# Optimization experiments

Measured on AMD Instinct MI355X. Metric: run time of the kernel, lower is better.

Reference implementation:

```python
import jax, jax.numpy as jnp
import numpy as np

EPS = 1e-7


def _project_to_ball(x, max_norm=0.9):
    # keep points strictly inside the unit Poincare ball
    n = jnp.linalg.norm(x, axis=-1, keepdims=True)
    return x * (max_norm / (1.0 + n))


def _poincare_pairwise_dist(x, y, c=1.0):
    # x: (B, d), y: (L, d) -> (B, L) hyperbolic distances
    x2 = jnp.sum(x * x, axis=-1, keepdims=True)            # (B, 1)
    y2 = jnp.sum(y * y, axis=-1, keepdims=True).T          # (1, L)
    xy = x @ y.T                                           # (B, L) GEMM
    sq = jnp.maximum(x2 + y2 - 2.0 * xy, 0.0)              # ||x - y||^2
    denom = jnp.maximum((1.0 - c * x2) * (1.0 - c * y2), EPS)
    arg = jnp.maximum(1.0 + 2.0 * c * sq / denom, 1.0 + EPS)
    return jnp.arccosh(arg) / jnp.sqrt(c)


def setup_inputs() -> dict:
    key = jax.random.key(0)
    k1, k2 = jax.random.split(key)
    z_hyp = _project_to_ball(jax.random.normal(k1, (4096, 256), dtype=jnp.float32))
    leaf_emb = _project_to_ball(jax.random.normal(k2, (50000, 256), dtype=jnp.float32))
    leaf_node_ids = jnp.arange(50000, dtype=jnp.int32)
    threshold = jnp.ones((), dtype=jnp.float32)
    return {"z_hyp": z_hyp, "leaf_emb": leaf_emb,
            "leaf_node_ids": leaf_node_ids, "threshold": threshold}


def reference(z_hyp, leaf_emb, leaf_node_ids, threshold):
    c = 1.0
    dists = _poincare_pairwise_dist(z_hyp, leaf_emb, c)      # (B, L)
    scores = jnp.min(dists, axis=-1)                          # (B,) OOD score
    is_ood = scores > threshold                               # (B,) bool
    k = min(5, leaf_emb.shape[0])
    # topk smallest distances -> negate and take top_k
    _, topk = jax.lax.top_k(-dists, k)                        # (B, 5)
    topk_ids = leaf_node_ids[topk]                            # (B, 5)
    return scores, is_ood, topk_ids
```

## Files before the change

kernel.cpp:

```cpp
#include <hip/hip_runtime.h>
#include <hip/hip_bf16.h>
#include <float.h>
#include <stdint.h>

#define BATCH 4096
#define NLEAF 50000
#define DIM   256
#define BN    128
#define NTILES 391
#define NGRP  (NTILES * 8)
#define MAXC  128
#define GCAP  2048
#define NCHUNK 8
#define GPC   ((NGRP + NCHUNK - 1) / NCHUNK)

typedef _Float16 h8  __attribute__((ext_vector_type(8)));
typedef float    f16v __attribute__((ext_vector_type(16)));
typedef unsigned long long u64;

__device__ __forceinline__ float h2f(unsigned short u) {
    return (float)__builtin_bit_cast(_Float16, u);
}

__device__ __forceinline__ void insert5v(float key, float (&k)[5]) {
    if (key < k[4]) {
        if (key < k[3]) { k[4]=k[3];
            if (key < k[2]) { k[3]=k[2];
                if (key < k[1]) { k[2]=k[1];
                    if (key < k[0]) { k[1]=k[0]; k[0]=key; } else k[1]=key;
                } else k[2]=key;
            } else k[3]=key;
        } else k[4]=key;
    }
}

__device__ __forceinline__ void insert5u(u64 key, u64 (&k)[5]) {
    if (key < k[4]) {
        if (key < k[3]) { k[4]=k[3];
            if (key < k[2]) { k[3]=k[2];
                if (key < k[1]) { k[2]=k[1];
                    if (key < k[0]) { k[1]=k[0]; k[0]=key; } else k[1]=key;
                } else k[2]=key;
            } else k[3]=key;
        } else k[4]=key;
    }
}

__device__ __forceinline__ bool lexless(float k, int i, float K, int I) {
    return (k < K) || (k == K && i < I);
}
__device__ __forceinline__ void insert5lex(float key, int id, float (&k)[5], int (&ix)[5]) {
    if (lexless(key, id, k[4], ix[4])) {
        if (lexless(key, id, k[3], ix[3])) { k[4]=k[3]; ix[4]=ix[3];
            if (lexless(key, id, k[2], ix[2])) { k[3]=k[2]; ix[3]=ix[2];
                if (lexless(key, id, k[1], ix[1])) { k[2]=k[1]; ix[2]=ix[1];
                    if (lexless(key, id, k[0], ix[0])) { k[1]=k[0]; ix[1]=ix[0]; k[0]=key; ix[0]=id; }
                    else { k[1]=key; ix[1]=id; }
                } else { k[2]=key; ix[2]=id; }
            } else { k[3]=key; ix[3]=id; }
        } else { k[4]=key; ix[4]=id; }
    }
}

__device__ __forceinline__ u64 umin64(u64 a, u64 b) { return a < b ? a : b; }
__device__ __forceinline__ u64 umax64(u64 a, u64 b) { return a > b ? a : b; }

__device__ __forceinline__ void gload_lds16(const void* g, void* l) {
    __builtin_amdgcn_global_load_lds(
        (const __attribute__((address_space(1))) uint32_t*)g,
        (__attribute__((address_space(3))) uint32_t*)l, 16, 0, 0);
}

__global__ void norms_cvt_k(const float* __restrict__ z, const float* __restrict__ leaf,
                            float* __restrict__ x2, float* __restrict__ afac,
                            float* __restrict__ y2, float* __restrict__ bfac,
                            unsigned short* __restrict__ zf, unsigned short* __restrict__ lf) {
    int wv = (blockIdx.x * 256 + threadIdx.x) >> 6;
    int l = threadIdx.x & 63;
    if (wv >= BATCH + NLEAF) return;
    bool isz = wv < BATCH;
    const float* row = isz ? z + (size_t)wv * DIM : leaf + (size_t)(wv - BATCH) * DIM;
    float4 v = reinterpret_cast<const float4*>(row)[l];
    _Float16 h0 = (_Float16)v.x, h1 = (_Float16)v.y, h2 = (_Float16)v.z, h3 = (_Float16)v.w;
    ushort4 u;
    u.x = __builtin_bit_cast(unsigned short, h0);
    u.y = __builtin_bit_cast(unsigned short, h1);
    u.z = __builtin_bit_cast(unsigned short, h2);
    u.w = __builtin_bit_cast(unsigned short, h3);
    unsigned short* dst = isz ? zf + (size_t)wv * DIM : lf + (size_t)(wv - BATCH) * DIM;
    reinterpret_cast<ushort4*>(dst)[l] = u;
    float s = v.x*v.x + v.y*v.y + v.z*v.z + v.w*v.w;
#pragma unroll
    for (int off = 32; off > 0; off >>= 1) s += __shfl_down(s, off, 64);
    if (l == 0) {
        if (isz) { x2[wv] = s; afac[wv] = 2.0f / (1.0f - s); }
        else { int j = wv - BATCH; y2[j] = s; bfac[j] = 1.0f / (1.0f - s); }
    }
}

__global__ __launch_bounds__(256, 2) void gemm_min_k(
        const unsigned short* __restrict__ zf, const unsigned short* __restrict__ lf,
        const float* __restrict__ x2, const float* __restrict__ y2,
        const float* __restrict__ bfac, unsigned short* __restrict__ mins) {
    extern __shared__ char sm[];
    float2* ybt = (float2*)(sm + 65536);
    float*  xt  = (float*)(sm + 66560);

    const int t = threadIdx.x;
    const int w = t >> 6, l = t & 63;
    const int wr = w >> 1, wc = w & 1;
    const int l31 = l & 31, lg2 = l >> 5;

    const int bid = blockIdx.x;
    const int xcd = bid & 7, q = bid >> 3;
    const int ntile = xcd * 49 + (q >> 5);
    if (ntile >= NTILES) return;
    const int m0 = (q & 31) * 128;
    const int l0 = ntile * BN;

    if (t < 128) {
        xt[t] = x2[m0 + t];
        int gl = l0 + t;
        bool v = gl < NLEAF;
        float bb = v ? bfac[gl] : 0.0f;
        float yy = v ? y2[gl] : 0.0f;
        ybt[t] = make_float2(bb, v ? yy * bb : 1e30f);
    }

    int srcA[4], srcB[4];
#pragma unroll
    for (int j = 0; j < 4; ++j) {
        int slot = j * 256 + t;
        int row = slot >> 3, sl = slot & 7;
        int swz = sl ^ (row & 7);
        srcA[j] = (m0 + row) * 512 + swz * 16;
        int gl = l0 + row; if (gl > NLEAF - 1) gl = NLEAF - 1;
        srcB[j] = gl * 512 + swz * 16;
    }

    f16v acc[2][2];
#pragma unroll
    for (int i = 0; i < 2; ++i)
#pragma unroll
        for (int j = 0; j < 2; ++j)
#pragma unroll
            for (int r = 0; r < 16; ++r) acc[i][j][r] = 0.0f;

    auto stage = [&](int ks, int bsel) {
        char* dst = sm + bsel * 32768;
        const int kb = ks * 128;
#pragma unroll
        for (int j = 0; j < 4; ++j) {
            gload_lds16((const char*)zf + srcA[j] + kb, dst + (j * 256 + w * 64) * 16);
            gload_lds16((const char*)lf + srcB[j] + kb, dst + 16384 + (j * 256 + w * 64) * 16);
        }
    };

    auto compute = [&](int bsel) {
        const char* Ab = sm + bsel * 32768;
        const char* Bb = Ab + 16384;
#pragma unroll
        for (int kk = 0; kk < 4; ++kk) {
            const int cz = kk * 32 + lg2 * 16;
            h8 za[2], lb[2];
#pragma unroll
            for (int f = 0; f < 2; ++f) {
                int ra = wr * 64 + f * 32 + l31;
                za[f] = *(const h8*)(Ab + ra * 128 + (cz ^ ((ra & 7) << 4)));
                int rb = wc * 64 + f * 32 + l31;
                lb[f] = *(const h8*)(Bb + rb * 128 + (cz ^ ((rb & 7) << 4)));
            }
#pragma unroll
            for (int fi = 0; fi < 2; ++fi)
#pragma unroll
                for (int fj = 0; fj < 2; ++fj)
                    acc[fi][fj] = __builtin_amdgcn_mfma_f32_32x32x16_f16(lb[fj], za[fi], acc[fi][fj], 0, 0, 0);
        }
    };

    stage(0, 0);
    __syncthreads();
#pragma unroll
    for (int ks = 0; ks < 4; ++ks) {
        if (ks < 3) stage(ks + 1, (ks + 1) & 1);
        compute(ks & 1);
        __syncthreads();
    }

    float xv[2] = { xt[wr * 64 + l31], xt[wr * 64 + 32 + l31] };
#pragma unroll
    for (int fi = 0; fi < 2; ++fi)
#pragma unroll
        for (int fj = 0; fj < 2; ++fj)
#pragma unroll
            for (int hi = 0; hi < 2; ++hi) {
                float kx[8];
#pragma unroll
                for (int r8 = 0; r8 < 8; ++r8) {
                    int reg = hi * 8 + r8;
                    int L = wc * 64 + fj * 32 + (r8 & 3) + 8 * (r8 >> 2) + 4 * lg2 + 16 * hi;
                    float2 p = ybt[L];
                    float a = acc[fi][fj][reg];
                    kx[r8] = fmaf(p.x, fmaf(-2.0f, a, xv[fi]), p.y);
                }
                float gm = fminf(fminf(fminf(kx[0], kx[1]), fminf(kx[2], kx[3])),
                                 fminf(fminf(kx[4], kx[5]), fminf(kx[6], kx[7])));
                gm = fminf(gm, __shfl_xor(gm, 32, 64));
                if (lg2 == 0) {
                    int g = ntile * 8 + wc * 4 + fj * 2 + hi;
                    _Float16 hgm = (_Float16)fminf(gm, 60000.0f);
                    mins[(size_t)g * BATCH + m0 + wr * 64 + fi * 32 + l31] =
                        __builtin_bit_cast(unsigned short, hgm);
                }
            }
}

__global__ __launch_bounds__(256) void select1_k(const unsigned short* __restrict__ mins,
                                                 float* __restrict__ part5) {
    __shared__ float sm5[4][64][5];
    const int w = threadIdx.x >> 6, l = threadIdx.x & 63;
    const int row = blockIdx.x * 64 + l;
    const int jb = w * ((GPC + 3) / 4);
    const int je = min(GPC, jb + (GPC + 3) / 4);
    float t5[5] = {FLT_MAX, FLT_MAX, FLT_MAX, FLT_MAX, FLT_MAX};
    int j = jb;
    for (; j + 4 <= je; j += 4) {
        int g = blockIdx.y * GPC + j;
        float a0 = (g     < NGRP) ? h2f(mins[(size_t)g * BATCH + row]) : FLT_MAX;
        float a1 = (g + 1 < NGRP) ? h2f(mins[(size_t)(g + 1) * BATCH + row]) : FLT_MAX;
        float a2 = (g + 2 < NGRP) ? h2f(mins[(size_t)(g + 2) * BATCH + row]) : FLT_MAX;
        float a3 = (g + 3 < NGRP) ? h2f(mins[(size_t)(g + 3) * BATCH + row]) : FLT_MAX;
        float m4 = fminf(fminf(a0, a1), fminf(a2, a3));
        if (m4 < t5[4]) {
            insert5v(a0, t5); insert5v(a1, t5); insert5v(a2, t5); insert5v(a3, t5);
        }
    }
    for (; j < je; ++j) {
        int g = blockIdx.y * GPC + j;
        float a = (g < NGRP) ? h2f(mins[(size_t)g * BATCH + row]) : FLT_MAX;
        insert5v(a, t5);
    }
#pragma unroll
    for (int q = 0; q < 5; ++q) sm5[w][l][q] = t5[q];
    __syncthreads();
    if (w == 0) {
#pragma unroll
        for (int ww = 1; ww < 4; ++ww)
#pragma unroll
            for (int q = 0; q < 5; ++q) insert5v(sm5[ww][l][q], t5);
#pragma unroll
        for (int q = 0; q < 5; ++q)
            part5[((size_t)row * NCHUNK + blockIdx.y) * 5 + q] = t5[q];
    }
}

__global__ void select_merge_k(const float* __restrict__ part5,
                               float* __restrict__ rowthr, int* __restrict__ cnt,
                               int* __restrict__ ovf, int* __restrict__ gcnt) {
    int idx = blockIdx.x * 256 + threadIdx.x;
    if (idx < NGRP) gcnt[idx] = 0;
    if (idx >= BATCH) return;
    int row = idx;
    float t5[5] = {FLT_MAX, FLT_MAX, FLT_MAX, FLT_MAX, FLT_MAX};
    const float* p = part5 + (size_t)row * NCHUNK * 5;
    for (int s = 0; s < NCHUNK * 5; ++s) insert5v(p[s], t5);
    rowthr[row] = t5[4] + 2e-3f * fabsf(t5[4]) + 1.8e-2f;
    cnt[row] = 0;
    ovf[row] = 0;
}

__global__ __launch_bounds__(256) void select_scan_k(const unsigned short* __restrict__ mins,
                                                     const float* __restrict__ rowthr,
                                                     int* __restrict__ cnt,
                                                     int* __restrict__ cand,
                                                     int* __restrict__ gcnt,
                                                     unsigned int* __restrict__ glist,
                                                     int* __restrict__ ovf) {
    const int w = threadIdx.x >> 6, l = threadIdx.x & 63;
    const int row = blockIdx.x * 64 + l;
    const float thr = rowthr[row];
    const int jb = w * ((GPC + 3) / 4);
    const int je = min(GPC, jb + (GPC + 3) / 4);
    for (int j = jb; j < je; ++j) {
        int g = blockIdx.y * GPC + j;
        if (g >= NGRP) break;
        float m = h2f(mins[(size_t)g * BATCH + row]);
        if (m <= thr) {
            int c = atomicAdd(&cnt[row], 1);
            if (c < MAXC) {
                cand[row * MAXC + c] = g;
                int s = atomicAdd(&gcnt[g], 1);
                if (s < GCAP) glist[(size_t)g * GCAP + s] = ((unsigned)row << 7) | (unsigned)c;
                else ovf[row] = 1;
            }
        }
    }
}

__global__ __launch_bounds__(256) void recheck_g_k(
        const float* __restrict__ z, const float* __restrict__ leaf,
        const float* __restrict__ x2, const float* __restrict__ y2,
        const float* __restrict__ bfac,
        const int* __restrict__ gcnt, const unsigned int* __restrict__ glist,
        float* __restrict__ keybuf) {
    const int g = blockIdx.x;
    int n = gcnt[g];
    if (n <= 0) return;
    if (n > GCAP) n = GCAP;
    const int t = threadIdx.x, w = t >> 6, l = t & 63;
    const int j = l & 15, q = l >> 4;
    float lr[64];
    const float* lrow = leaf + (size_t)(g * 16 + j) * DIM + q * 64;
#pragma unroll
    for (int tt = 0; tt < 16; ++tt) {
        float4 v = *(const float4*)(lrow + tt * 4);
        lr[tt * 4 + 0] = v.x; lr[tt * 4 + 1] = v.y;
        lr[tt * 4 + 2] = v.z; lr[tt * 4 + 3] = v.w;
    }
    const float yb = y2[g * 16 + j], bb = bfac[g * 16 + j];
    for (int i = w; i < n; i += 4) {
        unsigned int pk = glist[(size_t)g * GCAP + i];
        int row = (int)(pk >> 7), ci = (int)(pk & 127u);
        const float4* z4 = (const float4*)(z + (size_t)row * DIM) + q * 16;
        float d = 0.0f;
#pragma unroll
        for (int tt = 0; tt < 16; ++tt) {
            float4 v = z4[tt];
            d = fmaf(v.x, lr[tt * 4 + 0], d);
            d = fmaf(v.y, lr[tt * 4 + 1], d);
            d = fmaf(v.z, lr[tt * 4 + 2], d);
            d = fmaf(v.w, lr[tt * 4 + 3], d);
        }
        d += __shfl_xor(d, 16, 64);
        d += __shfl_xor(d, 32, 64);
        if (q == 0) {
            float sq = fmaxf(x2[row] + yb - 2.0f * d, 0.0f);
            keybuf[((size_t)row * MAXC + ci) * 16 + j] = sq * bb;
        }
    }
}

__global__ __launch_bounds__(256) void final_k(
        const float* __restrict__ keybuf, const int* __restrict__ cand,
        const int* __restrict__ cnt, const int* __restrict__ ovf,
        const float* __restrict__ afac, const int* __restrict__ ids,
        const float* __restrict__ thr, float* __restrict__ out) {
    const int t = threadIdx.x, w = t >> 6, l = t & 63;
    const int row = blockIdx.x * 4 + w;
    if (ovf[row]) return;
    int nc = cnt[row]; if (nc > MAXC) nc = MAXC;
    u64 t5[5] = {~0ull, ~0ull, ~0ull, ~0ull, ~0ull};
    const float* kb = keybuf + (size_t)row * MAXC * 16;
    const int* cr = cand + row * MAXC;
    for (int idx = l; idx < nc * 16; idx += 64) {
        int ci = idx >> 4, j = idx & 15;
        float key = kb[ci * 16 + j];
        unsigned int id = (unsigned)(cr[ci] * 16 + j);
        u64 pk = ((u64)__float_as_uint(key) << 32) | (u64)id;
        insert5u(pk, t5);
    }
#pragma unroll
    for (int s = 1; s < 64; s <<= 1) {
        u64 o[5];
#pragma unroll
        for (int qq = 0; qq < 5; ++qq) o[qq] = __shfl_xor(t5[qq], s, 64);
        u64 n0 = umin64(t5[0], o[0]);
        u64 n1 = umin64(umin64(t5[1], o[1]), umax64(t5[0], o[0]));
        u64 n2 = umin64(umin64(t5[2], o[2]),
                 umin64(umax64(t5[0], o[1]), umax64(t5[1], o[0])));
        u64 n3 = umin64(umin64(t5[3], o[3]),
                 umin64(umax64(t5[0], o[2]),
                 umin64(umax64(t5[1], o[1]), umax64(t5[2], o[0]))));
        u64 n4 = umin64(umin64(t5[4], o[4]),
                 umin64(umin64(umax64(t5[0], o[3]), umax64(t5[1], o[2])),
                        umin64(umax64(t5[2], o[1]), umax64(t5[3], o[0]))));
        t5[0]=n0; t5[1]=n1; t5[2]=n2; t5[3]=n3; t5[4]=n4;
    }
    if (l == 0) {
        float k0 = __uint_as_float((unsigned)(t5[0] >> 32));
        float u = k0 * afac[row];
        u = fmaxf(u, 1e-7f);
        float dd = log1pf(u + sqrtf(u * (u + 2.0f)));
        out[row] = dd;
        out[BATCH + row] = (dd > thr[0]) ? 1.0f : 0.0f;
#pragma unroll
        for (int qq = 0; qq < 5; ++qq)
            out[2 * BATCH + (size_t)row * 5 + qq] = (float)ids[(unsigned)(t5[qq] & 0xFFFFFFFFull)];
    }
}

__global__ __launch_bounds__(256) void recheck_fb_k(
        const float* __restrict__ z, const float* __restrict__ leaf,
        const float* __restrict__ x2, const float* __restrict__ y2,
        const float* __restrict__ bfac, const float* __restrict__ afac,
        const int* __restrict__ cnt, const int* __restrict__ cand,
        const int* __restrict__ ovf,
        const int* __restrict__ ids, const float* __restrict__ thr,
        float* __restrict__ out) {
    __shared__ float mk[20];
    __shared__ int   mi[20];
    const int row = blockIdx.x;
    if (ovf[row] == 0) return;
    const int t = threadIdx.x, w = t >> 6, l = t & 63;
    float4 zr = *(const float4*)(z + (size_t)row * DIM + l * 4);
    const float x2r = x2[row];
    int nc = cnt[row]; if (nc > MAXC) nc = MAXC;
    float k5[5]; int i5[5];
#pragma unroll
    for (int q = 0; q < 5; ++q) { k5[q] = FLT_MAX; i5[q] = 0x7FFFFFFF; }
    for (int ci = w; ci < nc; ci += 4) {
        int g = cand[row * MAXC + ci];
#pragma unroll 1
        for (int jj = 0; jj < 16; ++jj) {
            int id = g * 16 + jj;
            if (id >= NLEAF) break;
            float4 lfv = *(const float4*)(leaf + (size_t)id * DIM + l * 4);
            float d = zr.x * lfv.x;
            d = fmaf(zr.y, lfv.y, d); d = fmaf(zr.z, lfv.z, d); d = fmaf(zr.w, lfv.w, d);
#pragma unroll
            for (int s = 1; s < 64; s <<= 1) d += __shfl_xor(d, s, 64);
            float sq = fmaxf(x2r + y2[id] - 2.0f * d, 0.0f);
            float key = sq * bfac[id];
            insert5lex(key, id, k5, i5);
        }
    }
    if (l == 0) {
#pragma unroll
        for (int q = 0; q < 5; ++q) { mk[w * 5 + q] = k5[q]; mi[w * 5 + q] = i5[q]; }
    }
    __syncthreads();
    if (t == 0) {
        float fk[5]; int fi[5];
#pragma unroll
        for (int q = 0; q < 5; ++q) { fk[q] = FLT_MAX; fi[q] = 0x7FFFFFFF; }
        for (int s = 0; s < 20; ++s) insert5lex(mk[s], mi[s], fk, fi);
        float u = fk[0] * afac[row];
        u = fmaxf(u, 1e-7f);
        float dd = log1pf(u + sqrtf(u * (u + 2.0f)));
        out[row] = dd;
        out[BATCH + row] = (dd > thr[0]) ? 1.0f : 0.0f;
#pragma unroll
        for (int q = 0; q < 5; ++q)
            out[2 * BATCH + (size_t)row * 5 + q] = (float)ids[fi[q]];
    }
}

extern "C" void kernel_launch(void* const* d_in, const int* in_sizes, int n_in,
                              void* d_out, int out_size, void* d_ws, size_t ws_size,
                              hipStream_t stream) {
    const float* z    = (const float*)d_in[0];
    const float* leaf = (const float*)d_in[1];
    const int*   ids  = (const int*)d_in[2];
    const float* thr  = (const float*)d_in[3];
    float* out = (float*)d_out;

    char* ws = (char*)d_ws;
    float* x2   = (float*)(ws + 0);
    float* afac = (float*)(ws + 16384);
    float* y2   = (float*)(ws + 32768);
    float* bfac = (float*)(ws + 232768);
    unsigned short* zf = (unsigned short*)(ws + 432768);
    unsigned short* lf = (unsigned short*)(ws + 2529920);
    unsigned short* mins = (unsigned short*)(ws + 28129920);
    int* cnt  = (int*)(ws + 53754496);
    int* ovf  = (int*)(ws + 53770880);
    int* gcnt = (int*)(ws + 53787264);
    int* cand = (int*)(ws + 53803648);
    float* part5  = (float*)(ws + 55900800);
    float* rowthr = (float*)(ws + 56556160);
    unsigned int* glist = (unsigned int*)(ws + 56572544);
    float* keybuf = (float*)(ws + 432768);

    norms_cvt_k<<<(BATCH + NLEAF + 3) / 4, 256, 0, stream>>>(z, leaf, x2, afac, y2, bfac, zf, lf);
    gemm_min_k<<<8 * 49 * 32, 256, 67072, stream>>>(zf, lf, x2, y2, bfac, mins);
    select1_k<<<dim3(BATCH / 64, NCHUNK), 256, 0, stream>>>(mins, part5);
    select_merge_k<<<16, 256, 0, stream>>>(part5, rowthr, cnt, ovf, gcnt);
    select_scan_k<<<dim3(BATCH / 64, NCHUNK), 256, 0, stream>>>(mins, rowthr, cnt, cand, gcnt, glist, ovf);
    recheck_g_k<<<NGRP, 256, 0, stream>>>(z, leaf, x2, y2, bfac, gcnt, glist, keybuf);
    final_k<<<BATCH / 4, 256, 0, stream>>>(keybuf, cand, cnt, ovf, afac, ids, thr, out);
    recheck_fb_k<<<BATCH, 256, 0, stream>>>(z, leaf, x2, y2, bfac, afac, cnt, cand, ovf, ids, thr, out);
}
```

Measured before the change: 386.5 us.

## Fuse three selection kernels into one per-row-block kernel with LDS counters

```diff
diff --git a/kernel.cpp b/kernel.cpp
--- a/kernel.cpp
+++ b/kernel.cpp
@@ -11,8 +11,6 @@
 #define NGRP  (NTILES * 8)
 #define MAXC  128
 #define GCAP  2048
-#define NCHUNK 8
-#define GPC   ((NGRP + NCHUNK - 1) / NCHUNK)
 
 typedef _Float16 h8  __attribute__((ext_vector_type(8)));
 typedef float    f16v __attribute__((ext_vector_type(16)));
@@ -74,8 +72,11 @@
 __global__ void norms_cvt_k(const float* __restrict__ z, const float* __restrict__ leaf,
                             float* __restrict__ x2, float* __restrict__ afac,
                             float* __restrict__ y2, float* __restrict__ bfac,
-                            unsigned short* __restrict__ zf, unsigned short* __restrict__ lf) {
-    int wv = (blockIdx.x * 256 + threadIdx.x) >> 6;
+                            unsigned short* __restrict__ zf, unsigned short* __restrict__ lf,
+                            int* __restrict__ gcnt) {
+    int gid = blockIdx.x * 256 + threadIdx.x;
+    if (gid < NGRP) gcnt[gid] = 0;
+    int wv = gid >> 6;
     int l = threadIdx.x & 63;
     if (wv >= BATCH + NLEAF) return;
     bool isz = wv < BATCH;
@@ -215,85 +216,65 @@
             }
 }
 
-__global__ __launch_bounds__(256) void select1_k(const unsigned short* __restrict__ mins,
-                                                 float* __restrict__ part5) {
-    __shared__ float sm5[4][64][5];
-    const int w = threadIdx.x >> 6, l = threadIdx.x & 63;
-    const int row = blockIdx.x * 64 + l;
-    const int jb = w * ((GPC + 3) / 4);
-    const int je = min(GPC, jb + (GPC + 3) / 4);
+__global__ __launch_bounds__(1024) void selectfused_k(
+        const unsigned short* __restrict__ mins,
+        int* __restrict__ cnt, int* __restrict__ cand,
+        int* __restrict__ gcnt, unsigned int* __restrict__ glist,
+        int* __restrict__ ovf) {
+    __shared__ float sm5[16][64][5];
+    __shared__ float thr_s[64];
+    __shared__ int   cnt_s[64];
+    __shared__ int   ovf_s[64];
+    const int t = threadIdx.x, w = t >> 6, l = t & 63;
+    const int rb = blockIdx.x * 64;
+    const int row = rb + l;
+
     float t5[5] = {FLT_MAX, FLT_MAX, FLT_MAX, FLT_MAX, FLT_MAX};
-    int j = jb;
-    for (; j + 4 <= je; j += 4) {
-        int g = blockIdx.y * GPC + j;
-        float a0 = (g     < NGRP) ? h2f(mins[(size_t)g * BATCH + row]) : FLT_MAX;
-        float a1 = (g + 1 < NGRP) ? h2f(mins[(size_t)(g + 1) * BATCH + row]) : FLT_MAX;
-        float a2 = (g + 2 < NGRP) ? h2f(mins[(size_t)(g + 2) * BATCH + row]) : FLT_MAX;
-        float a3 = (g + 3 < NGRP) ? h2f(mins[(size_t)(g + 3) * BATCH + row]) : FLT_MAX;
+    for (int k4 = 0; k4 < 49; ++k4) {
+        int g0 = w + 64 * k4;
+        float a0 = (g0      < NGRP) ? h2f(mins[(size_t)g0 * BATCH + row]) : FLT_MAX;
+        float a1 = (g0 + 16 < NGRP) ? h2f(mins[(size_t)(g0 + 16) * BATCH + row]) : FLT_MAX;
+        float a2 = (g0 + 32 < NGRP) ? h2f(mins[(size_t)(g0 + 32) * BATCH + row]) : FLT_MAX;
+        float a3 = (g0 + 48 < NGRP) ? h2f(mins[(size_t)(g0 + 48) * BATCH + row]) : FLT_MAX;
         float m4 = fminf(fminf(a0, a1), fminf(a2, a3));
         if (m4 < t5[4]) {
             insert5v(a0, t5); insert5v(a1, t5); insert5v(a2, t5); insert5v(a3, t5);
         }
     }
-    for (; j < je; ++j) {
-        int g = blockIdx.y * GPC + j;
-        float a = (g < NGRP) ? h2f(mins[(size_t)g * BATCH + row]) : FLT_MAX;
-        insert5v(a, t5);
-    }
 #pragma unroll
     for (int q = 0; q < 5; ++q) sm5[w][l][q] = t5[q];
     __syncthreads();
+
     if (w == 0) {
-#pragma unroll
-        for (int ww = 1; ww < 4; ++ww)
-#pragma unroll
-            for (int q = 0; q < 5; ++q) insert5v(sm5[ww][l][q], t5);
-#pragma unroll
-        for (int q = 0; q < 5; ++q)
-            part5[((size_t)row * NCHUNK + blockIdx.y) * 5 + q] = t5[q];
-    }
-}
-
-__global__ void select_merge_k(const float* __restrict__ part5,
-                               float* __restrict__ rowthr, int* __restrict__ cnt,
-                               int* __restrict__ ovf, int* __restrict__ gcnt) {
-    int idx = blockIdx.x * 256 + threadIdx.x;
-    if (idx < NGRP) gcnt[idx] = 0;
-    if (idx >= BATCH) return;
-    int row = idx;
-    float t5[5] = {FLT_MAX, FLT_MAX, FLT_MAX, FLT_MAX, FLT_MAX};
-    const float* p = part5 + (size_t)row * NCHUNK * 5;
-    for (int s = 0; s < NCHUNK * 5; ++s) insert5v(p[s], t5);
-    rowthr[row] = t5[4] + 2e-3f * fabsf(t5[4]) + 1.8e-2f;
-    cnt[row] = 0;
-    ovf[row] = 0;
-}
-
-__global__ __launch_bounds__(256) void select_scan_k(const unsigned short* __restrict__ mins,
-                                                     const float* __restrict__ rowthr,
-                                                     int* __restrict__ cnt,
-                                                     int* __restrict__ cand,
-                                                     int* __restrict__ gcnt,
-                                                     unsigned int* __restrict__ glist,
-                                                     int* __restrict__ ovf) {
-    const int w = threadIdx.x >> 6, l = threadIdx.x & 63;
-    const int row = blockIdx.x * 64 + l;
-    const float thr = rowthr[row];
-    const int jb = w * ((GPC + 3) / 4);
-    const int je = min(GPC, jb + (GPC + 3) / 4);
-    for (int j = jb; j < je; ++j) {
-        int g = blockIdx.y * GPC + j;
+        float f5[5] = {FLT_MAX, FLT_MAX, FLT_MAX, FLT_MAX, FLT_MAX};
+        for (int ww = 0; ww < 16; ++ww)
+#pragma unroll
+            for (int q = 0; q < 5; ++q) insert5v(sm5[ww][l][q], f5);
+        thr_s[l] = f5[4] + 2e-3f * fabsf(f5[4]) + 1.8e-2f;
+        cnt_s[l] = 0;
+        ovf_s[l] = 0;
+    }
+    __syncthreads();
+
+    const float thr = thr_s[l];
+    for (int k = 0; k < 196; ++k) {
+        int g = w + 16 * k;
         if (g >= NGRP) break;
         float m = h2f(mins[(size_t)g * BATCH + row]);
         if (m <= thr) {
-            int c = atomicAdd(&cnt[row], 1);
+            int c = atomicAdd(&cnt_s[l], 1);
             if (c < MAXC) {
                 cand[row * MAXC + c] = g;
                 int s = atomicAdd(&gcnt[g], 1);
                 if (s < GCAP) glist[(size_t)g * GCAP + s] = ((unsigned)row << 7) | (unsigned)c;
-                else ovf[row] = 1;
+                else ovf_s[l] = 1;
             }
         }
+    }
+    __syncthreads();
+    if (w == 0) {
+        cnt[row] = cnt_s[l];
+        ovf[row] = ovf_s[l];
     }
 }
 
@@ -466,16 +447,12 @@
     int* ovf  = (int*)(ws + 53770880);
     int* gcnt = (int*)(ws + 53787264);
     int* cand = (int*)(ws + 53803648);
-    float* part5  = (float*)(ws + 55900800);
-    float* rowthr = (float*)(ws + 56556160);
     unsigned int* glist = (unsigned int*)(ws + 56572544);
     float* keybuf = (float*)(ws + 432768);
 
-    norms_cvt_k<<<(BATCH + NLEAF + 3) / 4, 256, 0, stream>>>(z, leaf, x2, afac, y2, bfac, zf, lf);
+    norms_cvt_k<<<(BATCH + NLEAF + 3) / 4, 256, 0, stream>>>(z, leaf, x2, afac, y2, bfac, zf, lf, gcnt);
     gemm_min_k<<<8 * 49 * 32, 256, 67072, stream>>>(zf, lf, x2, y2, bfac, mins);
-    select1_k<<<dim3(BATCH / 64, NCHUNK), 256, 0, stream>>>(mins, part5);
-    select_merge_k<<<16, 256, 0, stream>>>(part5, rowthr, cnt, ovf, gcnt);
-    select_scan_k<<<dim3(BATCH / 64, NCHUNK), 256, 0, stream>>>(mins, rowthr, cnt, cand, gcnt, glist, ovf);
+    selectfused_k<<<BATCH / 64, 1024, 0, stream>>>(mins, cnt, cand, gcnt, glist, ovf);
     recheck_g_k<<<NGRP, 256, 0, stream>>>(z, leaf, x2, y2, bfac, gcnt, glist, keybuf);
     final_k<<<BATCH / 4, 256, 0, stream>>>(keybuf, cand, cnt, ovf, afac, ids, thr, out);
     recheck_fb_k<<<BATCH, 256, 0, stream>>>(z, leaf, x2, y2, bfac, afac, cnt, cand, ovf, ids, thr, out);
```

New measurement: 393.3 us. No clear change (+1.8%).
